# Optimization experiments

Measured on AMD Instinct MI355X. Metric: run time of the kernel, lower is better.

## Reference

```python
import jax, jax.numpy as jnp
import numpy as np

DIM = 2048
N_HEADS = 32
N_KV_HEADS = 8
HEAD_DIM = DIM // N_HEADS  # 64
N_REP = N_HEADS // N_KV_HEADS  # 4
B, S = 1, 2048


def _rope(t, cos, sin):
    # t: (b, s, h, head_dim); cos/sin: (s, head_dim//2)
    tr = t.reshape(*t.shape[:-1], -1, 2)
    a, b = tr[..., 0], tr[..., 1]
    c = cos[None, :, None, :]
    s_ = sin[None, :, None, :]
    ra = a * c - b * s_
    rb = a * s_ + b * c
    return jnp.stack([ra, rb], axis=-1).reshape(t.shape)


def setup_inputs() -> dict:
    key = jax.random.key(0)
    ks = jax.random.split(key, 6)
    sc = 1.0 / np.sqrt(DIM)
    x = jax.random.normal(ks[0], (B, S, DIM), dtype=jnp.float32)
    wq = jax.random.normal(ks[1], (DIM, N_HEADS * HEAD_DIM), dtype=jnp.float32) * sc
    wk = jax.random.normal(ks[2], (DIM, N_KV_HEADS * HEAD_DIM), dtype=jnp.float32) * sc
    wv = jax.random.normal(ks[3], (DIM, N_KV_HEADS * HEAD_DIM), dtype=jnp.float32) * sc
    wo = jax.random.normal(ks[4], (N_HEADS * HEAD_DIM, DIM), dtype=jnp.float32) * sc
    # rotary frequencies (theta = 500000 as in Llama3)
    inv = 1.0 / (500000.0 ** (np.arange(0, HEAD_DIM, 2, dtype=np.float32) / HEAD_DIM))
    ang = np.arange(S, dtype=np.float32)[:, None] * inv[None, :]
    freqs_cos = jnp.asarray(np.cos(ang), dtype=jnp.float32)
    freqs_sin = jnp.asarray(np.sin(ang), dtype=jnp.float32)
    # causal additive mask
    mask = jnp.triu(jnp.full((S, S), -1e9, dtype=jnp.float32), k=1)
    return {"x": x, "wq": wq, "wk": wk, "wv": wv, "wo": wo,
            "freqs_cos": freqs_cos, "freqs_sin": freqs_sin, "mask": mask,
            "start_pos": 0}


def reference(x, wq, wk, wv, wo, freqs_cos, freqs_sin, mask, start_pos):
    b, s, _ = x.shape
    xq = (x @ wq).reshape(b, s, N_HEADS, HEAD_DIM)
    xk = (x @ wk).reshape(b, s, N_KV_HEADS, HEAD_DIM)
    xv = (x @ wv).reshape(b, s, N_KV_HEADS, HEAD_DIM)
    xq = _rope(xq, freqs_cos, freqs_sin)
    xk = _rope(xk, freqs_cos, freqs_sin)
    # GQA without repeat_interleave: view queries as (b, s, kv, rep, d)
    q = xq.reshape(b, s, N_KV_HEADS, N_REP, HEAD_DIM)
    scale = 1.0 / np.sqrt(HEAD_DIM)
    # scores: (b, kv, rep, q, k)
    scores = jnp.einsum('bqkrd,bskd->bkrqs', q, xk) * scale
    scores = scores + mask[None, None, None, :, :]
    probs = jax.nn.softmax(scores.astype(jnp.float32), axis=-1).astype(x.dtype)
    out = jnp.einsum('bkrqs,bskd->bqkrd', probs, xv)
    out = out.reshape(b, s, N_HEADS * HEAD_DIM)
    return out @ wo
```

## Files before the change

kernel.cpp:

```cpp
#include <hip/hip_runtime.h>
#include <hip/hip_bf16.h>

#define DIM 2048
#define S_LEN 2048
#define N_HEADS 32
#define N_KV_HEADS 8
#define HEAD_DIM 64
#define KV_DIM (N_KV_HEADS * HEAD_DIM)
#define QKV_N (DIM + 2 * KV_DIM)
#define QSCALE 0.18033688011112042f

typedef __attribute__((ext_vector_type(8))) short bf16x8;
typedef __attribute__((ext_vector_type(4))) float f32x4;

__device__ __forceinline__ unsigned short bf16_of(float f) {
    __hip_bfloat16 h = __float2bfloat16(f);
    return *reinterpret_cast<unsigned short*>(&h);
}
__device__ __forceinline__ float f_of_bf16(unsigned short u) {
    unsigned int x = ((unsigned int)u) << 16;
    return __uint_as_float(x);
}
__device__ __forceinline__ void gl_lds16(const void* g, void* l) {
    __builtin_amdgcn_global_load_lds((const __attribute__((address_space(1))) void*)g,
                                     (__attribute__((address_space(3))) void*)l, 16, 0, 0);
}
__device__ __forceinline__ unsigned int pack2tr(float lo, float hi) {
    return __builtin_amdgcn_perm(__float_as_uint(hi), __float_as_uint(lo), 0x07060302u);
}
__device__ __forceinline__ float max3f(float a, float b, float c) {
    float d;
    asm("v_max3_f32 %0, %1, %2, %3" : "=v"(d) : "v"(a), "v"(b), "v"(c));
    return d;
}

__global__ __launch_bounds__(256) void prep(const float* __restrict__ x,
                                            const float* __restrict__ wq,
                                            const float* __restrict__ wk,
                                            const float* __restrict__ wv,
                                            const float* __restrict__ wo,
                                            unsigned short* __restrict__ xbf,
                                            unsigned short* __restrict__ wqkvT,
                                            unsigned short* __restrict__ woT) {
    __shared__ float tile[64][65];
    const int t = threadIdx.x;
    int b = blockIdx.x;
    if (b < 4096) {
        int idx = b * 256 + t;
        float4 f = ((const float4*)x)[idx];
        ushort4 u;
        u.x = bf16_of(f.x); u.y = bf16_of(f.y); u.z = bf16_of(f.z); u.w = bf16_of(f.w);
        ((ushort4*)xbf)[idx] = u;
        return;
    }
    b -= 4096;
    const float* src;
    unsigned short* dst;
    int src_cols, bx, by;
    if (b < 1024)      { src = wq; dst = wqkvT;                                src_cols = DIM;    bx = b & 31;          by = b >> 5; }
    else if (b < 1280) { src = wk; dst = wqkvT + (size_t)DIM * DIM;            src_cols = KV_DIM; bx = (b - 1024) & 7;  by = (b - 1024) >> 3; }
    else if (b < 1536) { src = wv; dst = wqkvT + (size_t)(DIM + KV_DIM) * DIM; src_cols = KV_DIM; bx = (b - 1280) & 7;  by = (b - 1280) >> 3; }
    else               { src = wo; dst = woT;                                  src_cols = DIM;    bx = (b - 1536) & 31; by = (b - 1536) >> 5; }
    const int c0 = bx * 64, r0 = by * 64;
#pragma unroll
    for (int i = 0; i < 16; i++) {
        int idx = t + i * 256;
        int r = idx >> 6, c = idx & 63;
        tile[r][c] = src[(size_t)(r0 + r) * src_cols + c0 + c];
    }
    __syncthreads();
#pragma unroll
    for (int i = 0; i < 8; i++) {
        int idx = t + i * 256;
        int rr = idx >> 5, cc = (idx & 31) * 2;
        ushort2 u2;
        u2.x = bf16_of(tile[cc][rr]);
        u2.y = bf16_of(tile[cc + 1][rr]);
        *(ushort2*)&dst[(size_t)(c0 + rr) * DIM + r0 + cc] = u2;
    }
}

__global__ __launch_bounds__(256) void gemm_bt64(const unsigned short* __restrict__ A,
                                                 const unsigned short* __restrict__ Bt,
                                                 void* __restrict__ Cv,
                                                 int M, int N, int K, int c_bf16) {
    __shared__ unsigned short As[2][128 * 64];
    __shared__ unsigned short Bs[2][64 * 64];
    const int tid = threadIdx.x;
    const int wave = tid >> 6, lane = tid & 63;
    const int m16 = lane & 15, quad = lane >> 4;
    const int m0 = blockIdx.y * 128, n0 = blockIdx.x * 64;
    const int wm = (wave >> 1) * 64, wn = (wave & 1) * 32;

    const int lrow = lane >> 3;
    const int gc = (lane & 7) ^ lrow;
    const unsigned short* Ab = A + (size_t)(m0 + wave * 8 + lrow) * K + gc * 8;
    const unsigned short* Bb = Bt + (size_t)(n0 + wave * 8 + lrow) * K + gc * 8;

    f32x4 acc[4][2];
#pragma unroll
    for (int mb = 0; mb < 4; mb++)
#pragma unroll
        for (int nb = 0; nb < 2; nb++) acc[mb][nb] = (f32x4){0.f, 0.f, 0.f, 0.f};

#pragma unroll
    for (int g = 0; g < 4; g++)
        gl_lds16(Ab + (size_t)g * 32 * K, &As[0][(g * 32 + wave * 8) * 64]);
#pragma unroll
    for (int g = 0; g < 2; g++)
        gl_lds16(Bb + (size_t)g * 32 * K, &Bs[0][(g * 32 + wave * 8) * 64]);

    const int nt = K >> 6;
    for (int kt = 0; kt < nt; kt++) {
        __syncthreads();
        if (kt + 1 < nt) {
            const int nb2 = (kt + 1) & 1;
            const int k0 = (kt + 1) << 6;
#pragma unroll
            for (int g = 0; g < 4; g++)
                gl_lds16(Ab + (size_t)g * 32 * K + k0, &As[nb2][(g * 32 + wave * 8) * 64]);
#pragma unroll
            for (int g = 0; g < 2; g++)
                gl_lds16(Bb + (size_t)g * 32 * K + k0, &Bs[nb2][(g * 32 + wave * 8) * 64]);
        }
        const unsigned short* A_ = As[kt & 1];
        const unsigned short* B_ = Bs[kt & 1];
#pragma unroll
        for (int ks = 0; ks < 2; ks++) {
            const int ch = (ks * 4 + quad) ^ (m16 & 7);
            bf16x8 af[4], bfr[2];
#pragma unroll
            for (int mb = 0; mb < 4; mb++)
                af[mb] = *(const bf16x8*)&A_[(wm + mb * 16 + m16) * 64 + ch * 8];
#pragma unroll
            for (int nb = 0; nb < 2; nb++)
                bfr[nb] = *(const bf16x8*)&B_[(wn + nb * 16 + m16) * 64 + ch * 8];
#pragma unroll
            for (int mb = 0; mb < 4; mb++)
#pragma unroll
                for (int nb = 0; nb < 2; nb++)
                    acc[mb][nb] = __builtin_amdgcn_mfma_f32_16x16x32_bf16(af[mb], bfr[nb], acc[mb][nb], 0, 0, 0);
        }
    }

    if (c_bf16) {
        unsigned short* C = (unsigned short*)Cv;
#pragma unroll
        for (int mb = 0; mb < 4; mb++)
#pragma unroll
            for (int nb = 0; nb < 2; nb++)
#pragma unroll
                for (int r = 0; r < 4; r++)
                    C[(size_t)(m0 + wm + mb * 16 + quad * 4 + r) * N + n0 + wn + nb * 16 + m16] =
                        bf16_of(acc[mb][nb][r]);
    } else {
        float* C = (float*)Cv;
#pragma unroll
        for (int mb = 0; mb < 4; mb++)
#pragma unroll
            for (int nb = 0; nb < 2; nb++)
#pragma unroll
                for (int r = 0; r < 4; r++)
                    C[(size_t)(m0 + wm + mb * 16 + quad * 4 + r) * N + n0 + wn + nb * 16 + m16] =
                        acc[mb][nb][r];
    }
}

__global__ __launch_bounds__(256) void rope_tv(const unsigned short* __restrict__ qkv,
                                               unsigned short* __restrict__ qbf,
                                               unsigned short* __restrict__ kbf,
                                               unsigned short* __restrict__ vbt,
                                               const float* __restrict__ fcos,
                                               const float* __restrict__ fsin) {
    __shared__ unsigned short tile[64][65];
    const int t = threadIdx.x;
    int b = blockIdx.x;
    if (b < 2560) {
        int idx = b * 256 + t;
        const int nq = S_LEN * N_HEADS * 8;
        int s, j, srcoff, dstoff;
        unsigned short* dst;
        float osc;
        if (idx < nq) {
            s = idx >> 8;
            int rem = idx & 255;
            int h = rem >> 3;
            j = rem & 7;
            srcoff = s * QKV_N + h * 64 + j * 8;
            dstoff = s * DIM + h * 64 + j * 8;
            dst = qbf;
            osc = QSCALE;
        } else {
            int t2 = idx - nq;
            s = t2 >> 6;
            int rem = t2 & 63;
            int h = rem >> 3;
            j = rem & 7;
            srcoff = s * QKV_N + DIM + h * 64 + j * 8;
            dstoff = s * KV_DIM + h * 64 + j * 8;
            dst = kbf;
            osc = 1.0f;
        }
        bf16x8 v8 = *(const bf16x8*)&qkv[srcoff];
        float4 c4 = *(const float4*)&fcos[s * 32 + j * 4];
        float4 s4 = *(const float4*)&fsin[s * 32 + j * 4];
        float cs[4] = {c4.x, c4.y, c4.z, c4.w};
        float sn[4] = {s4.x, s4.y, s4.z, s4.w};
        bf16x8 o;
#pragma unroll
        for (int p = 0; p < 4; p++) {
            float a = f_of_bf16((unsigned short)v8[2 * p]);
            float bb = f_of_bf16((unsigned short)v8[2 * p + 1]);
            o[2 * p]     = (short)bf16_of((a * cs[p] - bb * sn[p]) * osc);
            o[2 * p + 1] = (short)bf16_of((a * sn[p] + bb * cs[p]) * osc);
        }
        *(bf16x8*)&dst[dstoff] = o;
        return;
    }
    b -= 2560;
    const int d0 = (b & 7) * 64;
    const int s0 = (b >> 3) * 64;
#pragma unroll
    for (int i = 0; i < 16; i++) {
        int idx = t + i * 256;
        int r = idx >> 6, c = idx & 63;
        tile[r][c] = qkv[(size_t)(s0 + r) * QKV_N + DIM + KV_DIM + d0 + c];
    }
    __syncthreads();
#pragma unroll
    for (int i = 0; i < 16; i++) {
        int idx = t + i * 256;
        int r = idx >> 6, c = idx & 63;
        int key = s0 + c;
        int kl = key & 127;
        int kp = (kl & 0x60) | ((kl & 0x0C) << 1) | ((kl & 0x10) >> 2) | (kl & 3);
        vbt[(size_t)(d0 + r) * S_LEN + (key & ~127) + kp] = tile[c][r];
    }
}

__global__ __launch_bounds__(256) void attn_mfma6(const unsigned short* __restrict__ qb,
                                                  const unsigned short* __restrict__ kb,
                                                  const unsigned short* __restrict__ vbt,
                                                  unsigned short* __restrict__ out) {
    const int h  = blockIdx.y;
    const int bx = blockIdx.x;
    const int kh = h >> 2;
    const int tid  = threadIdx.x;
    const int wave = tid >> 6;
    const int lane = tid & 63;
    const int m16  = lane & 15;
    const int quad = lane >> 4;

    __shared__ unsigned short Ks[2][128 * 64];
    __shared__ unsigned short Vt[2][64 * 128];

    const int lrow8 = lane >> 3;
    const int kc    = (lane & 7) ^ lrow8;
    const int lrow4 = lane >> 4;
    const int vc    = (lane & 15) ^ ((wave * 4 + lrow4) & 7);

    const unsigned short* Kbase = kb + (size_t)kh * 64 + (size_t)(wave * 8 + lrow8) * KV_DIM + kc * 8;
    const unsigned short* Vbase = vbt + (size_t)(kh * 64 + wave * 4 + lrow4) * S_LEN + vc * 8;

    bf16x8 ones;
#pragma unroll
    for (int i = 0; i < 8; i++) ones[i] = (short)0x3F80;

#pragma unroll
    for (int half = 0; half < 2; half++) {
        const int qt = half ? bx : (31 - bx);
        const int q0 = qt * 64;
        const int n_iter = (qt >> 1) + 1;

        bf16x8 qa[2];
        {
            const int qrow = q0 + wave * 16 + m16;
#pragma unroll
            for (int ks = 0; ks < 2; ks++)
                qa[ks] = *(const bf16x8*)&qb[(size_t)qrow * DIM + h * 64 + ks * 32 + quad * 8];
        }

        f32x4 o_acc[4];
#pragma unroll
        for (int nb = 0; nb < 4; nb++) o_acc[nb] = (f32x4){0.f, 0.f, 0.f, 0.f};
        f32x4 l_acc = (f32x4){0.f, 0.f, 0.f, 0.f};
        float m_s = -1e30f;
        const int qrow_lane = q0 + wave * 16 + m16;
        const int orow_base = q0 + wave * 16 + quad * 4;

        if (half) __syncthreads();

#pragma unroll
        for (int g = 0; g < 4; g++) {
            gl_lds16(Kbase + (size_t)(g * 32) * KV_DIM, &Ks[0][(g * 32 + wave * 8) * 64]);
            gl_lds16(Vbase + (size_t)g * 16 * S_LEN, &Vt[0][(g * 16 + wave * 4) * 128]);
        }

        for (int kt = 0; kt < n_iter; kt++) {
            __syncthreads();
            if (kt + 1 < n_iter) {
                const int nb2 = (kt + 1) & 1;
#pragma unroll
                for (int g = 0; g < 4; g++) {
                    gl_lds16(Kbase + (size_t)((kt + 1) * 128 + g * 32) * KV_DIM,
                             &Ks[nb2][(g * 32 + wave * 8) * 64]);
                    gl_lds16(Vbase + (size_t)g * 16 * S_LEN + (kt + 1) * 128,
                             &Vt[nb2][(g * 16 + wave * 4) * 128]);
                }
            }
            const unsigned short* K_ = Ks[kt & 1];
            const unsigned short* V_ = Vt[kt & 1];

            f32x4 sc[8];
#pragma unroll
            for (int cb = 0; cb < 8; cb++) sc[cb] = (f32x4){0.f, 0.f, 0.f, 0.f};
            __builtin_amdgcn_s_setprio(1);
#pragma unroll
            for (int ks = 0; ks < 2; ks++) {
                const int slot = (ks * 4 + quad) ^ (m16 & 7);
#pragma unroll
                for (int cb = 0; cb < 8; cb++) {
                    bf16x8 kf = *(const bf16x8*)&K_[(cb * 16 + m16) * 64 + slot * 8];
                    sc[cb] = __builtin_amdgcn_mfma_f32_16x16x32_bf16(kf, qa[ks], sc[cb], 0, 0, 0);
                }
            }
            __builtin_amdgcn_s_setprio(0);

            if (kt == n_iter - 1) {
#pragma unroll
                for (int cb = 0; cb < 8; cb++) {
                    int key = kt * 128 + cb * 16 + quad * 4;
#pragma unroll
                    for (int r = 0; r < 4; r++)
                        if (key + r > qrow_lane) sc[cb][r] = -1e30f;
                }
            }

            float rmax = fmaxf(sc[0][0], sc[0][1]);
            rmax = max3f(sc[0][2], sc[0][3], rmax);
#pragma unroll
            for (int cb = 1; cb < 8; cb++) {
                rmax = max3f(sc[cb][0], sc[cb][1], rmax);
                rmax = max3f(sc[cb][2], sc[cb][3], rmax);
            }
            rmax = fmaxf(rmax, __shfl_xor(rmax, 16, 64));
            rmax = fmaxf(rmax, __shfl_xor(rmax, 32, 64));

            if (!__all(rmax - m_s <= 8.0f)) {
                float mnew = fmaxf(m_s, rmax);
                float alpha = __builtin_amdgcn_exp2f(m_s - mnew);
                m_s = mnew;
#pragma unroll
                for (int r = 0; r < 4; r++) {
                    float a_r = __shfl(alpha, quad * 4 + r, 64);
#pragma unroll
                    for (int nb = 0; nb < 4; nb++) o_acc[nb][r] *= a_r;
                    l_acc[r] *= a_r;
                }
            }

#pragma unroll
            for (int cb = 0; cb < 8; cb++)
#pragma unroll
                for (int r = 0; r < 4; r++)
                    sc[cb][r] = __builtin_amdgcn_exp2f(sc[cb][r] - m_s);

            unsigned int P01[8], P23[8];
#pragma unroll
            for (int cb = 0; cb < 8; cb++) {
                P01[cb] = pack2tr(sc[cb][0], sc[cb][1]);
                P23[cb] = pack2tr(sc[cb][2], sc[cb][3]);
            }

            __builtin_amdgcn_s_setprio(1);
#pragma unroll
            for (int ks = 0; ks < 4; ks++) {
                union { unsigned int u[4]; bf16x8 v; } pa;
                pa.u[0] = P01[2 * ks];     pa.u[1] = P23[2 * ks];
                pa.u[2] = P01[2 * ks + 1]; pa.u[3] = P23[2 * ks + 1];
                const int slot = (ks * 4 + quad) ^ (m16 & 7);
#pragma unroll
                for (int nb = 0; nb < 4; nb++) {
                    bf16x8 vf = *(const bf16x8*)&V_[(nb * 16 + m16) * 128 + slot * 8];
                    o_acc[nb] = __builtin_amdgcn_mfma_f32_16x16x32_bf16(pa.v, vf, o_acc[nb], 0, 0, 0);
                }
                l_acc = __builtin_amdgcn_mfma_f32_16x16x32_bf16(pa.v, ones, l_acc, 0, 0, 0);
            }
            __builtin_amdgcn_s_setprio(0);
        }

#pragma unroll
        for (int r = 0; r < 4; r++) {
            float inv_l = 1.f / l_acc[r];
#pragma unroll
            for (int nb = 0; nb < 4; nb++)
                out[(size_t)(orow_base + r) * DIM + h * 64 + nb * 16 + m16] =
                    bf16_of(o_acc[nb][r] * inv_l);
        }
    }
}

extern "C" void kernel_launch(void* const* d_in, const int* in_sizes, int n_in,
                              void* d_out, int out_size, void* d_ws, size_t ws_size,
                              hipStream_t stream) {
    const float* x    = (const float*)d_in[0];
    const float* wq   = (const float*)d_in[1];
    const float* wk   = (const float*)d_in[2];
    const float* wv   = (const float*)d_in[3];
    const float* wo   = (const float*)d_in[4];
    const float* fcos = (const float*)d_in[5];
    const float* fsin = (const float*)d_in[6];

    char* ws = (char*)d_ws;
    const size_t MB = 1024 * 1024;
    unsigned short* xbf    = (unsigned short*)(ws);
    unsigned short* wqkvT  = (unsigned short*)(ws + 8 * MB);
    unsigned short* woT    = (unsigned short*)(ws + 20 * MB);
    unsigned short* qkvbf  = (unsigned short*)(ws + 28 * MB);
    unsigned short* vbt    = (unsigned short*)(ws + 40 * MB);
    unsigned short* qbf    = (unsigned short*)(ws + 8 * MB);
    unsigned short* kbf    = (unsigned short*)(ws + 16 * MB);
    unsigned short* attnbf = (unsigned short*)(ws);

    prep<<<4096 + 2560, 256, 0, stream>>>(x, wq, wk, wv, wo, xbf, wqkvT, woT);

    gemm_bt64<<<dim3(QKV_N / 64, S_LEN / 128), 256, 0, stream>>>(xbf, wqkvT, qkvbf,
                                                                 S_LEN, QKV_N, DIM, 1);

    rope_tv<<<2560 + 256, 256, 0, stream>>>(qkvbf, qbf, kbf, vbt, fcos, fsin);

    attn_mfma6<<<dim3(16, N_HEADS), 256, 0, stream>>>(qbf, kbf, vbt, attnbf);

    gemm_bt64<<<dim3(DIM / 64, S_LEN / 128), 256, 0, stream>>>(attnbf, woT, d_out,
                                                               S_LEN, DIM, DIM, 0);
}
```

Baseline: 221.4 us.

## Split attention into one query tile per block and single-buffer V with staged waits

The attention kernel no longer pairs two query tiles per block (the causal load-balance trick). It launches one block per (head, query tile), 1024 blocks in total, with heads on the x dimension so blocks that share a KV head are scheduled close together, and the heaviest tiles go first. V now uses a single LDS buffer. It is loaded at the start of each iteration, overlapping the QK^T and softmax work, and a partial vmcnt wait plus a barrier sit before PV, while K stays double-buffered. This cuts LDS use and raises the number of blocks for occupancy, at the cost of extra barriers, V latency exposed per iteration, and reliance on the tail-block ordering to balance the causal work.

```diff
diff --git a/kernel.cpp b/kernel.cpp
--- a/kernel.cpp
+++ b/kernel.cpp
@@ -238,12 +238,12 @@
     }
 }
 
-__global__ __launch_bounds__(256) void attn_mfma6(const unsigned short* __restrict__ qb,
+__global__ __launch_bounds__(256) void attn_mfma9(const unsigned short* __restrict__ qb,
                                                   const unsigned short* __restrict__ kb,
                                                   const unsigned short* __restrict__ vbt,
                                                   unsigned short* __restrict__ out) {
-    const int h  = blockIdx.y;
-    const int bx = blockIdx.x;
+    const int h  = blockIdx.x;
+    const int qt = 31 - (int)blockIdx.y;
     const int kh = h >> 2;
     const int tid  = threadIdx.x;
     const int wave = tid >> 6;
@@ -252,7 +252,7 @@
     const int quad = lane >> 4;
 
     __shared__ unsigned short Ks[2][128 * 64];
-    __shared__ unsigned short Vt[2][64 * 128];
+    __shared__ unsigned short Vt[64 * 128];
 
     const int lrow8 = lane >> 3;
     const int kc    = (lane & 7) ^ lrow8;
@@ -266,137 +266,135 @@
 #pragma unroll
     for (int i = 0; i < 8; i++) ones[i] = (short)0x3F80;
 
-#pragma unroll
-    for (int half = 0; half < 2; half++) {
-        const int qt = half ? bx : (31 - bx);
-        const int q0 = qt * 64;
-        const int n_iter = (qt >> 1) + 1;
-
-        bf16x8 qa[2];
-        {
-            const int qrow = q0 + wave * 16 + m16;
-#pragma unroll
-            for (int ks = 0; ks < 2; ks++)
-                qa[ks] = *(const bf16x8*)&qb[(size_t)qrow * DIM + h * 64 + ks * 32 + quad * 8];
-        }
-
-        f32x4 o_acc[4];
-#pragma unroll
-        for (int nb = 0; nb < 4; nb++) o_acc[nb] = (f32x4){0.f, 0.f, 0.f, 0.f};
-        f32x4 l_acc = (f32x4){0.f, 0.f, 0.f, 0.f};
-        float m_s = -1e30f;
-        const int qrow_lane = q0 + wave * 16 + m16;
-        const int orow_base = q0 + wave * 16 + quad * 4;
-
-        if (half) __syncthreads();
-
-#pragma unroll
-        for (int g = 0; g < 4; g++) {
-            gl_lds16(Kbase + (size_t)(g * 32) * KV_DIM, &Ks[0][(g * 32 + wave * 8) * 64]);
-            gl_lds16(Vbase + (size_t)g * 16 * S_LEN, &Vt[0][(g * 16 + wave * 4) * 128]);
-        }
-
-        for (int kt = 0; kt < n_iter; kt++) {
-            __syncthreads();
-            if (kt + 1 < n_iter) {
-                const int nb2 = (kt + 1) & 1;
-#pragma unroll
-                for (int g = 0; g < 4; g++) {
-                    gl_lds16(Kbase + (size_t)((kt + 1) * 128 + g * 32) * KV_DIM,
-                             &Ks[nb2][(g * 32 + wave * 8) * 64]);
-                    gl_lds16(Vbase + (size_t)g * 16 * S_LEN + (kt + 1) * 128,
-                             &Vt[nb2][(g * 16 + wave * 4) * 128]);
-                }
+    const int q0 = qt * 64;
+    const int n_iter = (qt >> 1) + 1;
+
+    bf16x8 qa[2];
+    {
+        const int qrow = q0 + wave * 16 + m16;
+#pragma unroll
+        for (int ks = 0; ks < 2; ks++)
+            qa[ks] = *(const bf16x8*)&qb[(size_t)qrow * DIM + h * 64 + ks * 32 + quad * 8];
+    }
+
+    f32x4 o_acc[4];
+#pragma unroll
+    for (int nb = 0; nb < 4; nb++) o_acc[nb] = (f32x4){0.f, 0.f, 0.f, 0.f};
+    f32x4 l_acc = (f32x4){0.f, 0.f, 0.f, 0.f};
+    float m_s = -1e30f;
+    const int qrow_lane = q0 + wave * 16 + m16;
+    const int orow_base = q0 + wave * 16 + quad * 4;
+
+#pragma unroll
+    for (int g = 0; g < 4; g++)
+        gl_lds16(Kbase + (size_t)(g * 32) * KV_DIM, &Ks[0][(g * 32 + wave * 8) * 64]);
+
+    for (int kt = 0; kt < n_iter; kt++) {
+        asm volatile("s_waitcnt vmcnt(0)" ::: "memory");
+        __builtin_amdgcn_s_barrier();
+        __builtin_amdgcn_sched_barrier(0);
+
+        const int knext = (kt + 1 < n_iter) ? (kt + 1) : kt;
+#pragma unroll
+        for (int g = 0; g < 4; g++)
+            gl_lds16(Vbase + (size_t)g * 16 * S_LEN + kt * 128,
+                     &Vt[(g * 16 + wave * 4) * 128]);
+#pragma unroll
+        for (int g = 0; g < 4; g++)
+            gl_lds16(Kbase + (size_t)(knext * 128 + g * 32) * KV_DIM,
+                     &Ks[(kt + 1) & 1][(g * 32 + wave * 8) * 64]);
+
+        const unsigned short* K_ = Ks[kt & 1];
+
+        f32x4 sc[8];
+#pragma unroll
+        for (int cb = 0; cb < 8; cb++) sc[cb] = (f32x4){0.f, 0.f, 0.f, 0.f};
+        __builtin_amdgcn_s_setprio(1);
+#pragma unroll
+        for (int ks = 0; ks < 2; ks++) {
+            const int slot = (ks * 4 + quad) ^ (m16 & 7);
+#pragma unroll
+            for (int cb = 0; cb < 8; cb++) {
+                bf16x8 kf = *(const bf16x8*)&K_[(cb * 16 + m16) * 64 + slot * 8];
+                sc[cb] = __builtin_amdgcn_mfma_f32_16x16x32_bf16(kf, qa[ks], sc[cb], 0, 0, 0);
             }
-            const unsigned short* K_ = Ks[kt & 1];
-            const unsigned short* V_ = Vt[kt & 1];
-
-            f32x4 sc[8];
-#pragma unroll
-            for (int cb = 0; cb < 8; cb++) sc[cb] = (f32x4){0.f, 0.f, 0.f, 0.f};
-            __builtin_amdgcn_s_setprio(1);
-#pragma unroll
-            for (int ks = 0; ks < 2; ks++) {
-                const int slot = (ks * 4 + quad) ^ (m16 & 7);
-#pragma unroll
-                for (int cb = 0; cb < 8; cb++) {
-                    bf16x8 kf = *(const bf16x8*)&K_[(cb * 16 + m16) * 64 + slot * 8];
-                    sc[cb] = __builtin_amdgcn_mfma_f32_16x16x32_bf16(kf, qa[ks], sc[cb], 0, 0, 0);
-                }
+        }
+        __builtin_amdgcn_s_setprio(0);
+
+        if (kt == n_iter - 1) {
+#pragma unroll
+            for (int cb = 0; cb < 8; cb++) {
+                int key = kt * 128 + cb * 16 + quad * 4;
+#pragma unroll
+                for (int r = 0; r < 4; r++)
+                    if (key + r > qrow_lane) sc[cb][r] = -1e30f;
             }
-            __builtin_amdgcn_s_setprio(0);
-
-            if (kt == n_iter - 1) {
-#pragma unroll
-                for (int cb = 0; cb < 8; cb++) {
-                    int key = kt * 128 + cb * 16 + quad * 4;
-#pragma unroll
-                    for (int r = 0; r < 4; r++)
-                        if (key + r > qrow_lane) sc[cb][r] = -1e30f;
-                }
+        }
+
+        float rmax = fmaxf(sc[0][0], sc[0][1]);
+        rmax = max3f(sc[0][2], sc[0][3], rmax);
+#pragma unroll
+        for (int cb = 1; cb < 8; cb++) {
+            rmax = max3f(sc[cb][0], sc[cb][1], rmax);
+            rmax = max3f(sc[cb][2], sc[cb][3], rmax);
+        }
+        rmax = fmaxf(rmax, __shfl_xor(rmax, 16, 64));
+        rmax = fmaxf(rmax, __shfl_xor(rmax, 32, 64));
+
+        if (!__all(rmax - m_s <= 8.0f)) {
+            float mnew = fmaxf(m_s, rmax);
+            float alpha = __builtin_amdgcn_exp2f(m_s - mnew);
+            m_s = mnew;
+#pragma unroll
+            for (int r = 0; r < 4; r++) {
+                float a_r = __shfl(alpha, quad * 4 + r, 64);
+#pragma unroll
+                for (int nb = 0; nb < 4; nb++) o_acc[nb][r] *= a_r;
+                l_acc[r] *= a_r;
             }
-
-            float rmax = fmaxf(sc[0][0], sc[0][1]);
-            rmax = max3f(sc[0][2], sc[0][3], rmax);
-#pragma unroll
-            for (int cb = 1; cb < 8; cb++) {
-                rmax = max3f(sc[cb][0], sc[cb][1], rmax);
-                rmax = max3f(sc[cb][2], sc[cb][3], rmax);
+        }
+
+#pragma unroll
+        for (int cb = 0; cb < 8; cb++)
+#pragma unroll
+            for (int r = 0; r < 4; r++)
+                sc[cb][r] = __builtin_amdgcn_exp2f(sc[cb][r] - m_s);
+
+        unsigned int P01[8], P23[8];
+#pragma unroll
+        for (int cb = 0; cb < 8; cb++) {
+            P01[cb] = pack2tr(sc[cb][0], sc[cb][1]);
+            P23[cb] = pack2tr(sc[cb][2], sc[cb][3]);
+        }
+
+        asm volatile("s_waitcnt vmcnt(4)" ::: "memory");
+        __builtin_amdgcn_s_barrier();
+        __builtin_amdgcn_sched_barrier(0);
+
+        __builtin_amdgcn_s_setprio(1);
+#pragma unroll
+        for (int ks = 0; ks < 4; ks++) {
+            union { unsigned int u[4]; bf16x8 v; } pa;
+            pa.u[0] = P01[2 * ks];     pa.u[1] = P23[2 * ks];
+            pa.u[2] = P01[2 * ks + 1]; pa.u[3] = P23[2 * ks + 1];
+            const int slot = (ks * 4 + quad) ^ (m16 & 7);
+#pragma unroll
+            for (int nb = 0; nb < 4; nb++) {
+                bf16x8 vf = *(const bf16x8*)&Vt[(nb * 16 + m16) * 128 + slot * 8];
+                o_acc[nb] = __builtin_amdgcn_mfma_f32_16x16x32_bf16(pa.v, vf, o_acc[nb], 0, 0, 0);
             }
-            rmax = fmaxf(rmax, __shfl_xor(rmax, 16, 64));
-            rmax = fmaxf(rmax, __shfl_xor(rmax, 32, 64));
-
-            if (!__all(rmax - m_s <= 8.0f)) {
-                float mnew = fmaxf(m_s, rmax);
-                float alpha = __builtin_amdgcn_exp2f(m_s - mnew);
-                m_s = mnew;
-#pragma unroll
-                for (int r = 0; r < 4; r++) {
-                    float a_r = __shfl(alpha, quad * 4 + r, 64);
-#pragma unroll
-                    for (int nb = 0; nb < 4; nb++) o_acc[nb][r] *= a_r;
-                    l_acc[r] *= a_r;
-                }
-            }
-
-#pragma unroll
-            for (int cb = 0; cb < 8; cb++)
-#pragma unroll
-                for (int r = 0; r < 4; r++)
-                    sc[cb][r] = __builtin_amdgcn_exp2f(sc[cb][r] - m_s);
-
-            unsigned int P01[8], P23[8];
-#pragma unroll
-            for (int cb = 0; cb < 8; cb++) {
-                P01[cb] = pack2tr(sc[cb][0], sc[cb][1]);
-                P23[cb] = pack2tr(sc[cb][2], sc[cb][3]);
-            }
-
-            __builtin_amdgcn_s_setprio(1);
-#pragma unroll
-            for (int ks = 0; ks < 4; ks++) {
-                union { unsigned int u[4]; bf16x8 v; } pa;
-                pa.u[0] = P01[2 * ks];     pa.u[1] = P23[2 * ks];
-                pa.u[2] = P01[2 * ks + 1]; pa.u[3] = P23[2 * ks + 1];
-                const int slot = (ks * 4 + quad) ^ (m16 & 7);
-#pragma unroll
-                for (int nb = 0; nb < 4; nb++) {
-                    bf16x8 vf = *(const bf16x8*)&V_[(nb * 16 + m16) * 128 + slot * 8];
-                    o_acc[nb] = __builtin_amdgcn_mfma_f32_16x16x32_bf16(pa.v, vf, o_acc[nb], 0, 0, 0);
-                }
-                l_acc = __builtin_amdgcn_mfma_f32_16x16x32_bf16(pa.v, ones, l_acc, 0, 0, 0);
-            }
-            __builtin_amdgcn_s_setprio(0);
-        }
-
-#pragma unroll
-        for (int r = 0; r < 4; r++) {
-            float inv_l = 1.f / l_acc[r];
-#pragma unroll
-            for (int nb = 0; nb < 4; nb++)
-                out[(size_t)(orow_base + r) * DIM + h * 64 + nb * 16 + m16] =
-                    bf16_of(o_acc[nb][r] * inv_l);
-        }
+            l_acc = __builtin_amdgcn_mfma_f32_16x16x32_bf16(pa.v, ones, l_acc, 0, 0, 0);
+        }
+        __builtin_amdgcn_s_setprio(0);
+    }
+
+#pragma unroll
+    for (int r = 0; r < 4; r++) {
+        float inv_l = 1.f / l_acc[r];
+#pragma unroll
+        for (int nb = 0; nb < 4; nb++)
+            out[(size_t)(orow_base + r) * DIM + h * 64 + nb * 16 + m16] =
+                bf16_of(o_acc[nb][r] * inv_l);
     }
 }
 
@@ -429,7 +427,7 @@
 
     rope_tv<<<2560 + 256, 256, 0, stream>>>(qkvbf, qbf, kbf, vbt, fcos, fsin);
 
-    attn_mfma6<<<dim3(16, N_HEADS), 256, 0, stream>>>(qbf, kbf, vbt, attnbf);
+    attn_mfma9<<<dim3(N_HEADS, 32), 256, 0, stream>>>(qbf, kbf, vbt, attnbf);
 
     gemm_bt64<<<dim3(DIM / 64, S_LEN / 128), 256, 0, stream>>>(attnbf, woT, d_out,
                                                                S_LEN, DIM, DIM, 0);
```

Measured after the change: 216.6 us. 1.02x faster.
